# Kernel optimization log

Measured on AMD Instinct MI355X. Metric: run time of the kernel, lower is better.

Reference implementation:

```python
import jax, jax.numpy as jnp
import numpy as np

B, S, HID, H = 4, 4096, 1024, 16
EPS = 1e-12  # F.normalize default eps


def setup_inputs() -> dict:
    key = jax.random.key(0)
    ks = jax.random.split(key, 3)
    def lin_w(k, shape, fan_in):
        return jax.random.normal(k, shape, jnp.float32) * (fan_in ** -0.5)
    return {
        "x": jax.random.normal(ks[0], (B, S, HID), jnp.float32),
        "Wqkv": lin_w(ks[1], (3 * HID, HID), HID),
        "bqkv": jnp.zeros((3 * HID,), jnp.float32),
        "Wz": lin_w(ks[2], (HID, HID), HID),
        "bz": jnp.zeros((HID,), jnp.float32),
        "temperature": jnp.ones((H, 1, 1), jnp.float32),
    }


def reference(x, Wqkv, bqkv, Wz, bz, temperature):
    b, s, hid = x.shape
    h = temperature.shape[0]
    dh = hid // h
    scale = jnp.sqrt(jnp.asarray(hid, x.dtype))
    # QKV projection -> [3, B, H, Dh, S] (channels-as-tokens layout)
    qkv = (x @ Wqkv.T + bqkv).reshape(b, s, 3, h, dh)
    qkv = jnp.transpose(qkv, (2, 0, 3, 4, 1))
    Q, K, V = qkv[0], qkv[1], qkv[2]
    # L2-normalize along sequence axis (last dim)
    Q = Q / jnp.maximum(jnp.linalg.norm(Q, axis=-1, keepdims=True), EPS)
    K = K / jnp.maximum(jnp.linalg.norm(K, axis=-1, keepdims=True), EPS)
    # Channel-channel scores [B, H, Dh, Dh], temperature broadcasts per head
    w = jnp.einsum('bhds,bhes->bhde', Q, K) / scale * temperature
    attn = jax.nn.softmax(w, axis=-1)
    out = jnp.einsum('bhde,bhes->bhds', attn, V)  # [B, H, Dh, S]
    out = jnp.transpose(out, (0, 3, 1, 2)).reshape(b, s, hid)
    return out @ Wz.T + bz
```

## Files before the change

kernel.cpp:

```cpp
#include <hip/hip_runtime.h>

#define DEVINL __device__ __forceinline__

#define BB 4
#define SS 4096
#define HIDD 1024
#define HH 16
#define DH 64
#define NQKV 3072
#define MM (BB * SS)

typedef __attribute__((ext_vector_type(8))) short bf16x8_t;
typedef __attribute__((ext_vector_type(4))) float f32x4_t;

typedef __attribute__((address_space(1))) const void GV;
typedef __attribute__((address_space(3))) void LV;

DEVINL void gload16(const void* g, void* l) {
  __builtin_amdgcn_global_load_lds((GV*)g, (LV*)l, 16, 0, 0);
}

DEVINL float bf2f(ushort u) {
  union { unsigned int i; float f; } v;
  v.i = ((unsigned int)u) << 16;
  return v.f;
}
DEVINL ushort f2bf(float f) {
  unsigned int u = __float_as_uint(f);
  u = (u + 0x7fffu + ((u >> 16) & 1u)) >> 16;
  return (ushort)u;
}

__global__ __launch_bounds__(256) void k_f2bf(const float* __restrict__ src,
                                              ushort* __restrict__ dst, int n4) {
  int i = blockIdx.x * 256 + threadIdx.x;
  if (i >= n4) return;
  float4 v = ((const float4*)src)[i];
  ushort4 o;
  o.x = f2bf(v.x); o.y = f2bf(v.y); o.z = f2bf(v.z); o.w = f2bf(v.w);
  ((ushort4*)dst)[i] = o;
}

template <int MODE, int MDIM, int NDIM, int KDIM>
__global__ __launch_bounds__(512, 2) void k_gemm8p(
    const ushort* __restrict__ A, const ushort* __restrict__ B,
    const float* __restrict__ bias, void* __restrict__ Cv,
    ushort* __restrict__ qT, ushort* __restrict__ vbuf) {
  __shared__ ushort As0[256 * 64];
  __shared__ ushort As1[256 * 64];
  __shared__ ushort Bs0[256 * 64];
  __shared__ ushort Bs1[256 * 64];
  __shared__ ushort Dmy[4096];
  constexpr int NT = KDIM >> 6;
  const int t = threadIdx.x;
  const int m0 = blockIdx.x * 256, n0 = blockIdx.y * 256;
  const int lane = t & 63, wid = t >> 6;
  const int wm = wid >> 2, wn = wid & 3;
  const int fr = lane & 15, g = lane >> 4;
  const int srow = t >> 3;
  const int schunk = ((t & 7) ^ (srow & 7)) * 8;
  const ushort* Ab = A + (size_t)(m0 + srow) * KDIM + schunk;
  const ushort* Bb = B + (size_t)(n0 + srow) * KDIM + schunk;

  f32x4_t acc[8][4] = {};
  bf16x8_t af[2][2], bfr[4][2];

#define STG(ls_, gb_, tile, hf)                                             \
  {                                                                         \
    if ((tile) < NT) {                                                      \
      gload16((gb_) + (size_t)((hf) * 128) * KDIM + (tile) * 64,            \
              (ls_) + ((hf) * 128 + wid * 8) * 64);                         \
      gload16((gb_) + (size_t)((hf) * 128 + 64) * KDIM + (tile) * 64,       \
              (ls_) + ((hf) * 128 + wid * 8 + 64) * 64);                    \
    } else {                                                                \
      gload16((gb_), Dmy + wid * 512);                                      \
      gload16((gb_), Dmy + wid * 512);                                      \
    }                                                                       \
  }

#define LDA(as_, q)                                                         \
  _Pragma("unroll") for (int ii = 0; ii < 2; ++ii)                          \
  _Pragma("unroll") for (int kk = 0; kk < 2; ++kk) {                        \
    int r = wm * 128 + ((q) * 2 + ii) * 16 + fr;                            \
    af[ii][kk] = *(const bf16x8_t*)&(as_)[r * 64 + (((kk * 4 + g) ^ (r & 7)) * 8)]; \
  }

#define LDB(bs_)                                                            \
  _Pragma("unroll") for (int ni = 0; ni < 4; ++ni)                          \
  _Pragma("unroll") for (int kk = 0; kk < 2; ++kk) {                        \
    int r = wn * 64 + ni * 16 + fr;                                         \
    bfr[ni][kk] = *(const bf16x8_t*)&(bs_)[r * 64 + (((kk * 4 + g) ^ (r & 7)) * 8)]; \
  }

#define MMA(q)                                                              \
  _Pragma("unroll") for (int kk = 0; kk < 2; ++kk)                          \
  _Pragma("unroll") for (int ii = 0; ii < 2; ++ii)                          \
  _Pragma("unroll") for (int ni = 0; ni < 4; ++ni)                          \
    acc[(q) * 2 + ii][ni] = __builtin_amdgcn_mfma_f32_16x16x32_bf16(        \
        af[ii][kk], bfr[ni][kk], acc[(q) * 2 + ii][ni], 0, 0, 0);

#define BAR1                                                                \
  __builtin_amdgcn_s_barrier();                                             \
  __builtin_amdgcn_s_setprio(1);

#define BAR2                                                                \
  __builtin_amdgcn_s_setprio(0);                                            \
  __builtin_amdgcn_s_barrier();

#define BAR2VM                                                              \
  __builtin_amdgcn_s_setprio(0);                                            \
  asm volatile("s_waitcnt vmcnt(4)" ::: "memory");                          \
  __builtin_amdgcn_s_barrier();                                             \
  __builtin_amdgcn_sched_barrier(0);

  STG(Bs0, Bb, 0, 0); STG(Bs0, Bb, 0, 1);
  STG(As0, Ab, 0, 0); STG(As0, Ab, 0, 1);
  STG(Bs1, Bb, 1, 0); STG(Bs1, Bb, 1, 1);
  asm volatile("s_waitcnt vmcnt(4)" ::: "memory");
  __builtin_amdgcn_s_barrier();
  __builtin_amdgcn_sched_barrier(0);

#pragma unroll
  for (int J = 0; J < (NT >> 1); ++J) {
    const int T0 = 2 * J, T1 = 2 * J + 1;
    LDA(As0, 0); LDB(Bs0); STG(As1, Ab, T1, 0);
    BAR1; MMA(0); BAR2;
    LDA(As0, 1); STG(As1, Ab, T1, 1);
    BAR1; MMA(1); BAR2;
    LDA(As0, 2); STG(Bs0, Bb, T0 + 2, 0);
    BAR1; MMA(2); BAR2;
    LDA(As0, 3); STG(Bs0, Bb, T0 + 2, 1);
    BAR1; MMA(3); BAR2VM;
    LDA(As1, 0); LDB(Bs1); STG(As0, Ab, T0 + 2, 0);
    BAR1; MMA(0); BAR2;
    LDA(As1, 1); STG(As0, Ab, T0 + 2, 1);
    BAR1; MMA(1); BAR2;
    LDA(As1, 2); STG(Bs1, Bb, T1 + 2, 0);
    BAR1; MMA(2); BAR2;
    LDA(As1, 3); STG(Bs1, Bb, T1 + 2, 1);
    BAR1; MMA(3); BAR2VM;
  }
#undef STG
#undef LDA
#undef LDB
#undef MMA
#undef BAR1
#undef BAR2
#undef BAR2VM

  __syncthreads();

  if (MODE == 1) {
#pragma unroll
    for (int ni = 0; ni < 4; ++ni) {
      int col = n0 + wn * 64 + ni * 16 + fr;
      float bv = bias[col];
#pragma unroll
      for (int mi = 0; mi < 8; ++mi) {
        int rowbase = m0 + wm * 128 + mi * 16 + g * 4;
#pragma unroll
        for (int j = 0; j < 4; ++j)
          ((float*)Cv)[(size_t)(rowbase + j) * NDIM + col] = acc[mi][ni][j] + bv;
      }
    }
  } else {
    const int colbase = n0 + wn * 64;
    if (colbase < 2048) {
      ushort* scr = (wid < 2 ? As0 : wid < 4 ? As1 : wid < 6 ? Bs0 : Bs1) +
                    (wid & 1) * 8192;
      const int tt = colbase >> 10;
      const int hh = (colbase >> 6) & 15;
      const int bb = m0 >> 12;
      const int sbase0 = (m0 & 4095) + wm * 128;
      const int ch = lane & 7, dq = lane >> 3;
      ushort* qbase = qT + (((size_t)tt * BB + bb) * HH + hh) * 64 * SS;
#pragma unroll
      for (int half = 0; half < 2; ++half) {
#pragma unroll
        for (int ni = 0; ni < 4; ++ni) {
          float bv = bias[colbase + ni * 16 + fr];
#pragma unroll
          for (int mi_ = 0; mi_ < 4; ++mi_) {
#pragma unroll
            for (int jp = 0; jp < 2; ++jp) {
              unsigned int lo = f2bf(acc[half * 4 + mi_][ni][jp * 2] + bv);
              unsigned int hi = f2bf(acc[half * 4 + mi_][ni][jp * 2 + 1] + bv);
              *(unsigned int*)&scr[(ni * 16 + fr) * 72 + mi_ * 16 + g * 4 + jp * 2] =
                  lo | (hi << 16);
            }
          }
        }
        asm volatile("s_waitcnt lgkmcnt(0)" ::: "memory");
#pragma unroll
        for (int dr = 0; dr < 8; ++dr) {
          int d = dr * 8 + dq;
          int4 v = *(const int4*)&scr[d * 72 + ch * 8];
          *(int4*)&qbase[(size_t)d * SS + sbase0 + half * 64 + ch * 8] = v;
        }
        asm volatile("s_waitcnt lgkmcnt(0)" ::: "memory");
      }
    } else {
#pragma unroll
      for (int ni = 0; ni < 4; ++ni) {
        int col = colbase + ni * 16 + fr;
        float bv = bias[col];
        int c = col - 2048;
#pragma unroll
        for (int mi = 0; mi < 8; ++mi) {
          int rowbase = m0 + wm * 128 + mi * 16 + g * 4;
          vbuf[(size_t)(rowbase + 0) * HIDD + c] = f2bf(acc[mi][ni][0] + bv);
          vbuf[(size_t)(rowbase + 1) * HIDD + c] = f2bf(acc[mi][ni][1] + bv);
          vbuf[(size_t)(rowbase + 2) * HIDD + c] = f2bf(acc[mi][ni][2] + bv);
          vbuf[(size_t)(rowbase + 3) * HIDD + c] = f2bf(acc[mi][ni][3] + bv);
        }
      }
    }
  }
}

__global__ __launch_bounds__(256) void k_gram(const ushort* __restrict__ qT,
                                              float* __restrict__ Wp8,
                                              float* __restrict__ sq8,
                                              float* __restrict__ sk8) {
  __shared__ ushort Qs[3][64 * 64];
  __shared__ ushort Ks[3][64 * 64];
  const int bh = blockIdx.x, p = blockIdx.y;
  const ushort* Qp = qT + (size_t)bh * 64 * SS + p * 512;
  const ushort* Kp = qT + (size_t)(BB * HH + bh) * 64 * SS + p * 512;
  const int t = threadIdx.x;
  const int lane = t & 63, w = t >> 6;
  const int fr = lane & 15, g = lane >> 4;
  const int rsub = lane >> 3;
  const int gcol = ((lane & 7) ^ rsub) * 8;

  f32x4_t acc[4] = {};
  float sqa = 0.f, ska = 0.f;

#define STGG(b_, sc_)                                                       \
  _Pragma("unroll") for (int i = 0; i < 2; ++i) {                           \
    int rg = w * 2 + i;                                                     \
    int row = rg * 8 + rsub;                                                \
    gload16(&Qp[(size_t)row * SS + (sc_) * 64 + gcol], &Qs[b_][rg * 512]);  \
    gload16(&Kp[(size_t)row * SS + (sc_) * 64 + gcol], &Ks[b_][rg * 512]);  \
  }

#define GCOMP(bc)                                                           \
  {                                                                         \
    bf16x8_t af[2], bq[4][2];                                               \
    _Pragma("unroll") for (int kk = 0; kk < 2; ++kk) {                      \
      int r = w * 16 + fr;                                                  \
      af[kk] = *(const bf16x8_t*)&Qs[bc][r * 64 + (((kk * 4 + g) ^ (r & 7)) * 8)]; \
    }                                                                       \
    _Pragma("unroll") for (int ni = 0; ni < 4; ++ni)                        \
    _Pragma("unroll") for (int kk = 0; kk < 2; ++kk) {                      \
      int r2 = ni * 16 + fr;                                                \
      bq[ni][kk] = *(const bf16x8_t*)&Ks[bc][r2 * 64 + (((kk * 4 + g) ^ (r2 & 7)) * 8)]; \
    }                                                                       \
    _Pragma("unroll") for (int kk = 0; kk < 2; ++kk)                        \
    _Pragma("unroll") for (int ni = 0; ni < 4; ++ni)                        \
      acc[ni] = __builtin_amdgcn_mfma_f32_16x16x32_bf16(af[kk], bq[ni][kk], acc[ni], 0, 0, 0); \
    _Pragma("unroll") for (int kk = 0; kk < 2; ++kk)                        \
    _Pragma("unroll") for (int e = 0; e < 8; ++e) {                         \
      float fq = bf2f((ushort)af[kk][e]);                                   \
      sqa += fq * fq;                                                       \
    }                                                                       \
    _Pragma("unroll") for (int ni = 0; ni < 4; ++ni)                        \
      if (ni == w)                                                          \
        _Pragma("unroll") for (int kk = 0; kk < 2; ++kk)                    \
        _Pragma("unroll") for (int e = 0; e < 8; ++e) {                     \
          float fk = bf2f((ushort)bq[ni][kk][e]);                           \
          ska += fk * fk;                                                   \
        }                                                                   \
  }

#define GWAIT(n_)                                                           \
  asm volatile("s_waitcnt vmcnt(" #n_ ")" ::: "memory");                    \
  __builtin_amdgcn_s_barrier();                                             \
  __builtin_amdgcn_sched_barrier(0);

  STGG(0, 0);
  STGG(1, 1);
  for (int sc = 0; sc < 6; ++sc) {
    STGG((sc + 2) % 3, sc + 2);
    GWAIT(8);
    GCOMP(sc % 3);
    __builtin_amdgcn_s_barrier();
  }
  GWAIT(4); GCOMP(0); __builtin_amdgcn_s_barrier();
  GWAIT(0); GCOMP(1);
#undef STGG
#undef GCOMP
#undef GWAIT

  sqa += __shfl_xor(sqa, 16, 64); sqa += __shfl_xor(sqa, 32, 64);
  ska += __shfl_xor(ska, 16, 64); ska += __shfl_xor(ska, 32, 64);
  const int bp = bh * 8 + p;
  if (g == 0) {
    sq8[bp * 64 + w * 16 + fr] = sqa;
    sk8[bp * 64 + w * 16 + fr] = ska;
  }
  float* wp = Wp8 + (size_t)bp * 4096;
#pragma unroll
  for (int ni = 0; ni < 4; ++ni)
#pragma unroll
    for (int j = 0; j < 4; ++j)
      wp[(w * 16 + g * 4 + j) * 64 + ni * 16 + fr] = acc[ni][j];
}

__global__ __launch_bounds__(256) void k_smx(const float* __restrict__ Wp8,
                                             const float* __restrict__ sq8,
                                             const float* __restrict__ sk8,
                                             const float* __restrict__ temperature,
                                             ushort* __restrict__ attnb) {
  __shared__ float attnf[64][65];
  __shared__ float iqL[64], ikL[64], invs[64];
  const int bh = blockIdx.x, h = bh & 15;
  const int t = threadIdx.x;
  if (t < 64) {
    float sq = 0.f, sk = 0.f;
#pragma unroll
    for (int p = 0; p < 8; ++p) {
      sq += sq8[(bh * 8 + p) * 64 + t];
      sk += sk8[(bh * 8 + p) * 64 + t];
    }
    iqL[t] = 1.0f / fmaxf(sqrtf(sq), 1e-12f);
    ikL[t] = 1.0f / fmaxf(sqrtf(sk), 1e-12f);
  }
  __syncthreads();
  float tscale = temperature[h] * (1.0f / 32.0f);
  for (int idx = t; idx < 4096; idx += 256) {
    int d = idx >> 6, e = idx & 63;
    float s = 0.f;
#pragma unroll
    for (int p = 0; p < 8; ++p) s += Wp8[(size_t)(bh * 8 + p) * 4096 + idx];
    attnf[d][e] = s * iqL[d] * ikL[e] * tscale;
  }
  __syncthreads();
  if (t < 64) {
    float m = -1e30f;
#pragma unroll 8
    for (int e = 0; e < 64; ++e) m = fmaxf(m, attnf[t][e]);
    float sum = 0.f;
#pragma unroll 8
    for (int e = 0; e < 64; ++e) {
      float v = __expf(attnf[t][e] - m);
      attnf[t][e] = v;
      sum += v;
    }
    invs[t] = 1.0f / sum;
  }
  __syncthreads();
  for (int idx = t; idx < 4096; idx += 256) {
    int d = idx >> 6, e = idx & 63;
    attnb[(size_t)bh * 4608 + d * 72 + e] = f2bf(attnf[d][e] * invs[d]);
  }
}

__global__ __launch_bounds__(256) void k_pv(const ushort* __restrict__ vbuf,
                                            const ushort* __restrict__ attnb,
                                            ushort* __restrict__ attnout) {
  __shared__ ushort Vs[3][64 * 64];
  const int bh = blockIdx.x, p = blockIdx.y;
  const int b = bh >> 4, h = bh & 15;
  const int t = threadIdx.x;
  const int lane = t & 63, w = t >> 6;
  const int fr = lane & 15, g = lane >> 4;
  const int rsub = lane >> 3;
  const int gcol = ((lane & 7) ^ rsub) * 8;

  bf16x8_t bfg[4][2];
#pragma unroll
  for (int ni = 0; ni < 4; ++ni)
#pragma unroll
    for (int kk = 0; kk < 2; ++kk)
      bfg[ni][kk] = *(const bf16x8_t*)&attnb[(size_t)bh * 4608 + (ni * 16 + fr) * 72 + (kk * 4 + g) * 8];

  const ushort* vb = vbuf + (size_t)(b * SS + p * 512) * HIDD + h * 64;
  ushort* ob = attnout + (size_t)(b * SS + p * 512) * HIDD + h * 64;

#define STGV(b_, c_)                                                        \
  _Pragma("unroll") for (int i = 0; i < 2; ++i) {                           \
    int rg = w * 2 + i;                                                     \
    int row = rg * 8 + rsub;                                                \
    gload16(&vb[(size_t)((c_) * 64 + row) * HIDD + gcol], &Vs[b_][rg * 512]); \
  }

#define PCOMP(bc, c_)                                                       \
  {                                                                         \
    f32x4_t acc[4] = {};                                                    \
    _Pragma("unroll") for (int kk = 0; kk < 2; ++kk) {                      \
      int r = w * 16 + fr;                                                  \
      bf16x8_t af = *(const bf16x8_t*)&Vs[bc][r * 64 + (((kk * 4 + g) ^ (r & 7)) * 8)]; \
      _Pragma("unroll") for (int ni = 0; ni < 4; ++ni)                      \
        acc[ni] = __builtin_amdgcn_mfma_f32_16x16x32_bf16(af, bfg[ni][kk], acc[ni], 0, 0, 0); \
    }                                                                       \
    _Pragma("unroll") for (int ni = 0; ni < 4; ++ni)                        \
    _Pragma("unroll") for (int j = 0; j < 4; ++j)                           \
      ob[(size_t)((c_) * 64 + w * 16 + g * 4 + j) * HIDD + ni * 16 + fr] = f2bf(acc[ni][j]); \
  }

#define PWAIT(n_)                                                           \
  asm volatile("s_waitcnt vmcnt(" #n_ ")" ::: "memory");                    \
  __builtin_amdgcn_s_barrier();                                             \
  __builtin_amdgcn_sched_barrier(0);

  STGV(0, 0);
  STGV(1, 1);
  for (int c = 0; c < 6; ++c) {
    STGV((c + 2) % 3, c + 2);
    PWAIT(4);
    PCOMP(c % 3, c);
    __builtin_amdgcn_s_barrier();
  }
  PWAIT(2); PCOMP(0, 6); __builtin_amdgcn_s_barrier();
  PWAIT(0); PCOMP(1, 7);
#undef STGV
#undef PCOMP
#undef PWAIT
}

extern "C" void kernel_launch(void* const* d_in, const int* in_sizes, int n_in,
                              void* d_out, int out_size, void* d_ws, size_t ws_size,
                              hipStream_t stream) {
  const float* x = (const float*)d_in[0];
  const float* Wqkv = (const float*)d_in[1];
  const float* bqkv = (const float*)d_in[2];
  const float* Wz = (const float*)d_in[3];
  const float* bz = (const float*)d_in[4];
  const float* temperature = (const float*)d_in[5];

  char* ws = (char*)d_ws;
  ushort* xb    = (ushort*)(ws + 0);
  ushort* wqb   = (ushort*)(ws + 33554432);
  ushort* wzb   = (ushort*)(ws + 39845888);
  ushort* vbuf  = (ushort*)(ws + 41943040);
  ushort* qkvT  = (ushort*)(ws + 75497472);
  ushort* attnout = xb;

  float* dsc = (float*)d_out;
  float* Wp8 = dsc;
  float* sq8 = dsc + 2097152;
  float* sk8 = dsc + 2097152 + 32768;
  ushort* attnb = (ushort*)(dsc + 2097152 + 65536);

  k_f2bf<<<dim3(16384), dim3(256), 0, stream>>>(x, xb, (MM * HIDD) / 4);
  k_f2bf<<<dim3(3072), dim3(256), 0, stream>>>(Wqkv, wqb, (NQKV * HIDD) / 4);
  k_f2bf<<<dim3(1024), dim3(256), 0, stream>>>(Wz, wzb, (HIDD * HIDD) / 4);

  k_gemm8p<2, MM, NQKV, HIDD><<<dim3(MM / 256, NQKV / 256), dim3(512), 0, stream>>>(
      xb, wqb, bqkv, nullptr, qkvT, vbuf);

  k_gram<<<dim3(64, 8), dim3(256), 0, stream>>>(qkvT, Wp8, sq8, sk8);
  k_smx<<<dim3(64), dim3(256), 0, stream>>>(Wp8, sq8, sk8, temperature, attnb);

  k_pv<<<dim3(64, 8), dim3(256), 0, stream>>>(vbuf, attnb, attnout);

  k_gemm8p<1, MM, HIDD, HIDD><<<dim3(MM / 256, HIDD / 256), dim3(512), 0, stream>>>(
      attnout, wzb, bz, d_out, nullptr, nullptr);
}
```

Measured before the change: 215.5 us.

## Halve GEMM phase barriers and merge three bf16 conversion launches into one

The GEMM main loop goes from two barriers per MMA phase to one. Raised priority now wraps only the MFMA block, and the vmcnt wait sits in its own fence. The three fp32-to-bf16 conversion kernels are merged into a single launch that indexes across the contiguous workspace holding x, Wqkv and Wz. This removes barrier stalls and two kernel launches, but with fewer barriers LDS reads and global-to-LDS writes to the same buffer may now overlap, which is a correctness risk.

Result: faster. 209.9 us (-2.6%).

```diff
diff --git a/kernel.cpp b/kernel.cpp
--- a/kernel.cpp
+++ b/kernel.cpp
@@ -31,11 +31,17 @@
   return (ushort)u;
 }
 
-__global__ __launch_bounds__(256) void k_f2bf(const float* __restrict__ src,
-                                              ushort* __restrict__ dst, int n4) {
+__global__ __launch_bounds__(256) void k_f2bf3(const float* __restrict__ x,
+                                               const float* __restrict__ wq,
+                                               const float* __restrict__ wz,
+                                               ushort* __restrict__ dst) {
   int i = blockIdx.x * 256 + threadIdx.x;
-  if (i >= n4) return;
-  float4 v = ((const float4*)src)[i];
+  const float* src;
+  int off;
+  if (i < 4194304) { src = x; off = i; }
+  else if (i < 4980736) { src = wq; off = i - 4194304; }
+  else { src = wz; off = i - 4980736; }
+  float4 v = ((const float4*)src)[off];
   ushort4 o;
   o.x = f2bf(v.x); o.y = f2bf(v.y); o.z = f2bf(v.z); o.w = f2bf(v.w);
   ((ushort4*)dst)[i] = o;
@@ -99,54 +105,53 @@
     acc[(q) * 2 + ii][ni] = __builtin_amdgcn_mfma_f32_16x16x32_bf16(        \
         af[ii][kk], bfr[ni][kk], acc[(q) * 2 + ii][ni], 0, 0, 0);
 
-#define BAR1                                                                \
-  __builtin_amdgcn_s_barrier();                                             \
-  __builtin_amdgcn_s_setprio(1);
-
-#define BAR2                                                                \
-  __builtin_amdgcn_s_setprio(0);                                            \
-  __builtin_amdgcn_s_barrier();
-
-#define BAR2VM                                                              \
-  __builtin_amdgcn_s_setprio(0);                                            \
-  asm volatile("s_waitcnt vmcnt(4)" ::: "memory");                          \
+#define PHBAR                                                               \
   __builtin_amdgcn_s_barrier();                                             \
   __builtin_amdgcn_sched_barrier(0);
+
+#define MMAP(q)                                                             \
+  __builtin_amdgcn_s_setprio(1);                                            \
+  MMA(q);                                                                   \
+  __builtin_amdgcn_s_setprio(0);
+
+#define VMFENCE                                                             \
+  asm volatile("s_waitcnt vmcnt(4)" ::: "memory");                          \
+  PHBAR;
 
   STG(Bs0, Bb, 0, 0); STG(Bs0, Bb, 0, 1);
   STG(As0, Ab, 0, 0); STG(As0, Ab, 0, 1);
   STG(Bs1, Bb, 1, 0); STG(Bs1, Bb, 1, 1);
-  asm volatile("s_waitcnt vmcnt(4)" ::: "memory");
-  __builtin_amdgcn_s_barrier();
-  __builtin_amdgcn_sched_barrier(0);
+  VMFENCE;
 
 #pragma unroll
   for (int J = 0; J < (NT >> 1); ++J) {
     const int T0 = 2 * J, T1 = 2 * J + 1;
     LDA(As0, 0); LDB(Bs0); STG(As1, Ab, T1, 0);
-    BAR1; MMA(0); BAR2;
+    PHBAR; MMAP(0);
     LDA(As0, 1); STG(As1, Ab, T1, 1);
-    BAR1; MMA(1); BAR2;
+    PHBAR; MMAP(1);
     LDA(As0, 2); STG(Bs0, Bb, T0 + 2, 0);
-    BAR1; MMA(2); BAR2;
+    PHBAR; MMAP(2);
     LDA(As0, 3); STG(Bs0, Bb, T0 + 2, 1);
-    BAR1; MMA(3); BAR2VM;
+    PHBAR; MMAP(3);
+    VMFENCE;
     LDA(As1, 0); LDB(Bs1); STG(As0, Ab, T0 + 2, 0);
-    BAR1; MMA(0); BAR2;
+    PHBAR; MMAP(0);
     LDA(As1, 1); STG(As0, Ab, T0 + 2, 1);
-    BAR1; MMA(1); BAR2;
+    PHBAR; MMAP(1);
     LDA(As1, 2); STG(Bs1, Bb, T1 + 2, 0);
-    BAR1; MMA(2); BAR2;
+    PHBAR; MMAP(2);
     LDA(As1, 3); STG(Bs1, Bb, T1 + 2, 1);
-    BAR1; MMA(3); BAR2VM;
+    PHBAR; MMAP(3);
+    VMFENCE;
   }
 #undef STG
 #undef LDA
 #undef LDB
 #undef MMA
-#undef BAR1
-#undef BAR2
-#undef BAR2VM
+#undef MMAP
+#undef PHBAR
+#undef VMFENCE
 
   __syncthreads();
 
@@ -443,9 +448,7 @@
   float* sk8 = dsc + 2097152 + 32768;
   ushort* attnb = (ushort*)(dsc + 2097152 + 65536);
 
-  k_f2bf<<<dim3(16384), dim3(256), 0, stream>>>(x, xb, (MM * HIDD) / 4);
-  k_f2bf<<<dim3(3072), dim3(256), 0, stream>>>(Wqkv, wqb, (NQKV * HIDD) / 4);
-  k_f2bf<<<dim3(1024), dim3(256), 0, stream>>>(Wz, wzb, (HIDD * HIDD) / 4);
+  k_f2bf3<<<dim3(20480), dim3(256), 0, stream>>>(x, Wqkv, Wz, xb);
 
   k_gemm8p<2, MM, NQKV, HIDD><<<dim3(MM / 256, NQKV / 256), dim3(512), 0, stream>>>(
       xb, wqb, bqkv, nullptr, qkvT, vbuf);
```
